# Kernel optimization log

Hardware: AMD Instinct MI355X
Metric: run time of the kernel (lower is better)

The kernel has to match this reference:

```python
import jax, jax.numpy as jnp
import numpy as np

NUM_FEATURES = 64
SCALE = 10.0


def setup_inputs() -> dict:
    key = jax.random.key(0)
    k1, k2, k3, k4 = jax.random.split(key, 4)
    fractions = jax.random.uniform(k1, (4, 1024), dtype=jnp.float32)
    W = jax.random.normal(k2, (1, NUM_FEATURES), dtype=jnp.float32) * 0.1
    b = jax.random.uniform(k3, (NUM_FEATURES,), dtype=jnp.float32) * (2.0 * np.pi)
    a = jax.random.normal(k4, (NUM_FEATURES,), dtype=jnp.float32)
    return {"fractions": fractions, "W": W, "b": b, "a": a}


def reference(fractions, W, b, a):
    # diffs: [B, N, N]
    diffs = fractions[:, None, :] - fractions[:, :, None]
    scaled = diffs * SCALE
    # rff: [B, N, N, F] = cos(scaled[..., None] * W[0] + b)
    rff = jnp.cos(scaled[..., None] * W[0] + b)
    # weighted reduction over features -> [B, N, N]
    positional_bias = jnp.einsum("bijf,f->bij", rff, a)
    return positional_bias
```

## Files before the change

kernel.cpp:

```cpp
#include <hip/hip_runtime.h>
#include <hip/hip_bf16.h>

#define NPOS   1024
#define NBATCH 4
#define BT     64
#define LDT    136

typedef _Float16 half8  __attribute__((ext_vector_type(8)));
typedef _Float16 half2x __attribute__((ext_vector_type(2)));
typedef float    floatx4 __attribute__((ext_vector_type(4)));

#define INV2PI 0.15915494309189535f

__global__ __launch_bounds__(256, 4)
void fourier_bias_kernel(const float* __restrict__ frac,
                         const float* __restrict__ Wv,
                         const float* __restrict__ bv,
                         const float* __restrict__ av,
                         float* __restrict__ out) {
    __shared__ _Float16 sA[BT][LDT];
    __shared__ _Float16 sB[BT][LDT];

    const int tid = threadIdx.x;
    const int bz  = blockIdx.z;
    const int ti  = blockIdx.y * BT;
    const int tj  = blockIdx.x * BT;

    const int   f      = tid & 63;
    const int   rt     = tid >> 6;
    const float wf_rev = Wv[f] * (10.0f * INV2PI);
    const float bf_rev = bv[f] * INV2PI;
    const float af     = av[f];
    const float* fb = frac + bz * NPOS;

    #pragma unroll
    for (int t = 0; t < 16; ++t) {
        const int row = rt + t * 4;
        const float xi = fb[ti + row];
        const float ai = xi * wf_rev;
        half2x pa;
        pa[0] = (_Float16)__builtin_amdgcn_cosf(ai);
        pa[1] = (_Float16)__builtin_amdgcn_sinf(ai);
        *reinterpret_cast<half2x*>(&sA[row][2 * f]) = pa;
        const float xj = fb[tj + row];
        const float aj = __builtin_fmaf(xj, wf_rev, bf_rev);
        half2x pb;
        pb[0] = (_Float16)(af * __builtin_amdgcn_cosf(aj));
        pb[1] = (_Float16)(af * __builtin_amdgcn_sinf(aj));
        *reinterpret_cast<half2x*>(&sB[row][2 * f]) = pb;
    }
    __syncthreads();

    const int lane = tid & 63;
    const int wid  = tid >> 6;
    const int wr   = (wid >> 1) * 32;
    const int wc   = (wid & 1) * 32;

    const int lrow = lane & 15;
    const int lkb  = lane >> 4;

    floatx4 acc[2][2];
    #pragma unroll
    for (int m = 0; m < 2; ++m)
        #pragma unroll
        for (int n = 0; n < 2; ++n)
            acc[m][n] = (floatx4){0.f, 0.f, 0.f, 0.f};

    #pragma unroll
    for (int t = 0; t < 4; ++t) {
        const int k = t * 32 + lkb * 8;
        half8 afr[2], bfr[2];
        #pragma unroll
        for (int m = 0; m < 2; ++m)
            afr[m] = *reinterpret_cast<const half8*>(&sA[wr + m * 16 + lrow][k]);
        #pragma unroll
        for (int n = 0; n < 2; ++n)
            bfr[n] = *reinterpret_cast<const half8*>(&sB[wc + n * 16 + lrow][k]);
        #pragma unroll
        for (int m = 0; m < 2; ++m)
            #pragma unroll
            for (int n = 0; n < 2; ++n)
                acc[m][n] = __builtin_amdgcn_mfma_f32_16x16x32_f16(
                    afr[m], bfr[n], acc[m][n], 0, 0, 0);
    }

    const int col  = lane & 15;
    const int row4 = (lane >> 4) * 4;
    #pragma unroll
    for (int m = 0; m < 2; ++m) {
        #pragma unroll
        for (int n = 0; n < 2; ++n) {
            const size_t gi = (size_t)(ti + wr + m * 16 + row4);
            const size_t gj = (size_t)(tj + wc + n * 16 + col);
            float* o = out + ((size_t)bz * NPOS + gi) * NPOS + gj;
            #pragma unroll
            for (int r = 0; r < 4; ++r)
                o[(size_t)r * NPOS] = acc[m][n][r];
        }
    }
}

extern "C" void kernel_launch(void* const* d_in, const int* in_sizes, int n_in,
                              void* d_out, int out_size, void* d_ws, size_t ws_size,
                              hipStream_t stream) {
    const float* frac = (const float*)d_in[0];
    const float* Wv   = (const float*)d_in[1];
    const float* bv   = (const float*)d_in[2];
    const float* av   = (const float*)d_in[3];
    float* out = (float*)d_out;

    dim3 grid(NPOS / BT, NPOS / BT, NBATCH);
    fourier_bias_kernel<<<grid, dim3(256), 0, stream>>>(frac, Wv, bv, av, out);
}
```

Measured before the change: 11.75 us.

## Enlarge tile to 128x128 and stage output through LDS for vectorized nontemporal stores

Doubles the output tile per block to 128x128 so each block computes more MFMAs per sin/cos feature evaluation, cutting redundant transcendental work. B fragments are held in registers and reused across four row subtiles. The output is staged through a per-wave LDS buffer so each lane writes contiguous 16-byte nontemporal vector stores. Fractions are first loaded into LDS. The grid shrinks to 256 blocks with a larger LDS footprint, which lowers occupancy and may leave some compute units idle.

```diff
diff --git a/kernel.cpp b/kernel.cpp
--- a/kernel.cpp
+++ b/kernel.cpp
@@ -3,8 +3,9 @@
 
 #define NPOS   1024
 #define NBATCH 4
-#define BT     64
+#define RT     128
 #define LDT    136
+#define CLD    68
 
 typedef _Float16 half8  __attribute__((ext_vector_type(8)));
 typedef _Float16 half2x __attribute__((ext_vector_type(2)));
@@ -12,38 +13,42 @@
 
 #define INV2PI 0.15915494309189535f
 
-__global__ __launch_bounds__(256, 4)
+__global__ __launch_bounds__(256, 1)
 void fourier_bias_kernel(const float* __restrict__ frac,
                          const float* __restrict__ Wv,
                          const float* __restrict__ bv,
                          const float* __restrict__ av,
                          float* __restrict__ out) {
-    __shared__ _Float16 sA[BT][LDT];
-    __shared__ _Float16 sB[BT][LDT];
+    __shared__ _Float16 sA[RT][LDT];
+    __shared__ _Float16 sB[RT][LDT];
+    __shared__ float    sC[4][16][CLD];
+    __shared__ float    sXA[RT], sXB[RT];
 
     const int tid = threadIdx.x;
     const int bz  = blockIdx.z;
-    const int ti  = blockIdx.y * BT;
-    const int tj  = blockIdx.x * BT;
+    const int ti  = blockIdx.y * RT;
+    const int tj  = blockIdx.x * RT;
+
+    const float* fb = frac + bz * NPOS;
+    if (tid < 128) sXA[tid]       = fb[ti + tid];
+    else           sXB[tid - 128] = fb[tj + (tid - 128)];
 
     const int   f      = tid & 63;
-    const int   rt     = tid >> 6;
+    const int   rt4    = tid >> 6;
     const float wf_rev = Wv[f] * (10.0f * INV2PI);
     const float bf_rev = bv[f] * INV2PI;
     const float af     = av[f];
-    const float* fb = frac + bz * NPOS;
+    __syncthreads();
 
     #pragma unroll
-    for (int t = 0; t < 16; ++t) {
-        const int row = rt + t * 4;
-        const float xi = fb[ti + row];
-        const float ai = xi * wf_rev;
+    for (int t = 0; t < 32; ++t) {
+        const int row = rt4 + t * 4;
+        const float ai = sXA[row] * wf_rev;
         half2x pa;
         pa[0] = (_Float16)__builtin_amdgcn_cosf(ai);
         pa[1] = (_Float16)__builtin_amdgcn_sinf(ai);
         *reinterpret_cast<half2x*>(&sA[row][2 * f]) = pa;
-        const float xj = fb[tj + row];
-        const float aj = __builtin_fmaf(xj, wf_rev, bf_rev);
+        const float aj = __builtin_fmaf(sXB[row], wf_rev, bf_rev);
         half2x pb;
         pb[0] = (_Float16)(af * __builtin_amdgcn_cosf(aj));
         pb[1] = (_Float16)(af * __builtin_amdgcn_sinf(aj));
@@ -53,49 +58,51 @@
 
     const int lane = tid & 63;
     const int wid  = tid >> 6;
-    const int wr   = (wid >> 1) * 32;
-    const int wc   = (wid & 1) * 32;
-
+    const int wr   = (wid >> 1) * 64;
+    const int wc   = (wid & 1) * 64;
     const int lrow = lane & 15;
     const int lkb  = lane >> 4;
+    const int rhi  = (lane >> 4) * 4;
 
-    floatx4 acc[2][2];
+    half8 bfr[4][4];
     #pragma unroll
-    for (int m = 0; m < 2; ++m)
+    for (int t = 0; t < 4; ++t)
         #pragma unroll
-        for (int n = 0; n < 2; ++n)
-            acc[m][n] = (floatx4){0.f, 0.f, 0.f, 0.f};
+        for (int n = 0; n < 4; ++n)
+            bfr[t][n] = *reinterpret_cast<const half8*>(
+                &sB[wc + n * 16 + lrow][t * 32 + lkb * 8]);
 
     #pragma unroll
-    for (int t = 0; t < 4; ++t) {
-        const int k = t * 32 + lkb * 8;
-        half8 afr[2], bfr[2];
+    for (int m = 0; m < 4; ++m) {
+        floatx4 acc[4];
         #pragma unroll
-        for (int m = 0; m < 2; ++m)
-            afr[m] = *reinterpret_cast<const half8*>(&sA[wr + m * 16 + lrow][k]);
+        for (int n = 0; n < 4; ++n) acc[n] = (floatx4){0.f, 0.f, 0.f, 0.f};
+
         #pragma unroll
-        for (int n = 0; n < 2; ++n)
-            bfr[n] = *reinterpret_cast<const half8*>(&sB[wc + n * 16 + lrow][k]);
+        for (int t = 0; t < 4; ++t) {
+            const half8 afr = *reinterpret_cast<const half8*>(
+                &sA[wr + m * 16 + lrow][t * 32 + lkb * 8]);
+            #pragma unroll
+            for (int n = 0; n < 4; ++n)
+                acc[n] = __builtin_amdgcn_mfma_f32_16x16x32_f16(
+                    afr, bfr[t][n], acc[n], 0, 0, 0);
+        }
+
         #pragma unroll
-        for (int m = 0; m < 2; ++m)
-            #pragma unroll
-            for (int n = 0; n < 2; ++n)
-                acc[m][n] = __builtin_amdgcn_mfma_f32_16x16x32_f16(
-                    afr[m], bfr[n], acc[m][n], 0, 0, 0);
-    }
-
-    const int col  = lane & 15;
-    const int row4 = (lane >> 4) * 4;
-    #pragma unroll
-    for (int m = 0; m < 2; ++m) {
-        #pragma unroll
-        for (int n = 0; n < 2; ++n) {
-            const size_t gi = (size_t)(ti + wr + m * 16 + row4);
-            const size_t gj = (size_t)(tj + wc + n * 16 + col);
-            float* o = out + ((size_t)bz * NPOS + gi) * NPOS + gj;
+        for (int n = 0; n < 4; ++n)
             #pragma unroll
             for (int r = 0; r < 4; ++r)
-                o[(size_t)r * NPOS] = acc[m][n][r];
+                sC[wid][rhi + r][n * 16 + lrow] = acc[n][r];
+
+        #pragma unroll
+        for (int q = 0; q < 4; ++q) {
+            const int row16 = q * 4 + (lane >> 4);
+            const int c4    = lrow * 4;
+            const floatx4 v = *reinterpret_cast<const floatx4*>(&sC[wid][row16][c4]);
+            const size_t gi = (size_t)(ti + wr + m * 16 + row16);
+            const size_t gj = (size_t)(tj + wc + c4);
+            __builtin_nontemporal_store(
+                v, reinterpret_cast<floatx4*>(out + ((size_t)bz * NPOS + gi) * NPOS + gj));
         }
     }
 }
@@ -109,6 +116,6 @@
     const float* av   = (const float*)d_in[3];
     float* out = (float*)d_out;
 
-    dim3 grid(NPOS / BT, NPOS / BT, NBATCH);
+    dim3 grid(NPOS / RT, NPOS / RT, NBATCH);
     fourier_bias_kernel<<<grid, dim3(256), 0, stream>>>(frac, Wv, bv, av, out);
 }
```

Result: faster. 11.22 us, median of 2 (-4.5%).
